# Performance work log

Hardware: AMD Instinct MI355X
Metric: run time of the kernel (lower is better)

## Reference

```python
import jax, jax.numpy as jnp
import numpy as np

N_NODES = 100000
N_EDGES = 1600000
IN_CH = 1024
FEAT_CH = 128
OUT_CH = 3


def setup_inputs() -> dict:
    key = jax.random.key(0)
    ks = jax.random.split(key, 9)
    features = jax.random.normal(ks[0], (N_NODES, IN_CH), dtype=jnp.float32)
    edges = jax.random.randint(ks[1], (2, N_EDGES), 0, N_NODES, dtype=jnp.int64)
    edges2 = jax.random.randint(ks[2], (2, N_EDGES), 0, N_NODES, dtype=jnp.int64)
    edge_features = jax.random.normal(ks[3], (N_EDGES, 1), dtype=jnp.float32)
    additional_feature = jax.random.normal(ks[4], (N_NODES, 20), dtype=jnp.float32)
    # GCNConv linear weights (glorot-ish scale) and biases
    W1 = jax.random.normal(ks[5], (IN_CH, FEAT_CH), dtype=jnp.float32) * (1.0 / np.sqrt(IN_CH))
    b1 = jnp.zeros((FEAT_CH,), dtype=jnp.float32)
    W2 = jax.random.normal(ks[6], (FEAT_CH, OUT_CH), dtype=jnp.float32) * (1.0 / np.sqrt(FEAT_CH))
    b2 = jnp.zeros((OUT_CH,), dtype=jnp.float32)
    return {"features": features, "edges": edges, "edges2": edges2,
            "edge_features": edge_features, "additional_feature": additional_feature,
            "W1": W1, "b1": b1, "W2": W2, "b2": b2}


def gcn_conv(x, edge_index, W, b, num_nodes):
    """PyG GCNConv: x' = D^{-1/2}(A+I)D^{-1/2} x W + b (self-loops added)."""
    x = x @ W  # project first (cheaper feature dim for aggregation)
    loop = jnp.arange(num_nodes, dtype=edge_index.dtype)
    src = jnp.concatenate([edge_index[0], loop])
    dst = jnp.concatenate([edge_index[1], loop])
    deg = jax.ops.segment_sum(jnp.ones_like(dst, dtype=x.dtype), dst,
                              num_segments=num_nodes)  # >=1 due to self-loops
    dinv = jax.lax.rsqrt(deg)
    norm = dinv[src] * dinv[dst]  # [E+N]
    out = jax.ops.segment_sum(x[src] * norm[:, None], dst, num_segments=num_nodes)
    return out + b


def reference(features, edges, edges2, edge_features, additional_feature, W1, b1, W2, b2):
    # use_additional_channels=False -> features unchanged; edge_features forced to None
    n = features.shape[0]
    x = gcn_conv(features, edges2, W1, b1, n)
    x = jax.nn.relu(x)
    # dropout inactive in eval mode
    return gcn_conv(x, edges2, W2, b2, n)
```

## Files before the change

kernel.cpp:

```cpp
#include <hip/hip_runtime.h>
#include <hip/hip_bf16.h>

typedef __attribute__((ext_vector_type(8))) _Float16 half8;
typedef __attribute__((ext_vector_type(4))) _Float16 half4;
typedef __attribute__((ext_vector_type(4))) float f32x4;

#define N_NODES 100000
#define N_EDGES 1600000
#define IN_CH 1024
#define FEAT 128
#define CAP 64
#define NDIG 196
#define CAPC 10240
#define MROWS 16
#define NGB (N_NODES / MROWS)

__device__ __forceinline__ int swzA(int row, int kbyte) {
    return row * 2048 + (kbyte ^ ((row & 7) << 4) ^ (((kbyte >> 8) & 7) << 4));
}

__global__ void k_prep(const float* __restrict__ W1, _Float16* __restrict__ Bf,
                       int* __restrict__ cursorC, int* __restrict__ done) {
    int idx = blockIdx.x * 256 + threadIdx.x;
    if (idx < IN_CH * FEAT) {
        int col = idx & (FEAT - 1), k = idx >> 7;
        int ct = col >> 4, ks = k >> 5;
        int lane = ((k >> 3) & 3) * 16 + (col & 15);
        int e = k & 7;
        Bf[(((ct * 32 + ks) * 64 + lane) << 3) + e] = (_Float16)W1[idx];
    }
    if (idx < NDIG) cursorC[idx] = idx * CAPC;
    if (idx == 0) *done = 0;
}

__global__ __launch_bounds__(256, 4) void k_build_gemm(
    const float* __restrict__ A, const _Float16* __restrict__ Bf,
    const int4* __restrict__ src4, const int4* __restrict__ dst4,
    int* __restrict__ cursorC, uint2* __restrict__ recs,
    int* __restrict__ csr, int* __restrict__ cnt, float* __restrict__ dinvarr,
    int* __restrict__ done, _Float16* __restrict__ H, int M, int e4)
{
    __shared__ union {
        _Float16 As[MROWS * IN_CH];
        struct { int hist[NDIG], segoff[NDIG], lcur[NDIG]; } bin;
        int cl[512];
    } sm;
    const int t = threadIdx.x;

    if (blockIdx.x < NDIG) {
        const int b = blockIdx.x;
        if (t < NDIG) sm.bin.hist[t] = 0;
        __syncthreads();
        const int base4 = b * 2048;
        int4 sv[8], dv[8];
#pragma unroll
        for (int j = 0; j < 8; ++j) {
            int idx = base4 + j * 256 + t;
            if (idx < e4) { sv[j] = src4[idx]; dv[j] = dst4[idx]; }
            else { sv[j] = (int4){-1,-1,-1,-1}; dv[j] = (int4){-1,-1,-1,-1}; }
        }
#pragma unroll
        for (int j = 0; j < 8; ++j) {
            int dd[4] = {dv[j].x, dv[j].y, dv[j].z, dv[j].w};
            int ss[4] = {sv[j].x, sv[j].y, sv[j].z, sv[j].w};
#pragma unroll
            for (int c = 0; c < 4; ++c)
                if ((unsigned)dd[c] < N_NODES && (unsigned)ss[c] < N_NODES)
                    atomicAdd(&sm.bin.hist[dd[c] >> 9], 1);
        }
        __syncthreads();
        if (t < NDIG) {
            sm.bin.segoff[t] = atomicAdd(&cursorC[t], sm.bin.hist[t]);
            sm.bin.lcur[t] = 0;
        }
        __syncthreads();
#pragma unroll
        for (int j = 0; j < 8; ++j) {
            int dd[4] = {dv[j].x, dv[j].y, dv[j].z, dv[j].w};
            int ss[4] = {sv[j].x, sv[j].y, sv[j].z, sv[j].w};
#pragma unroll
            for (int c = 0; c < 4; ++c) {
                if ((unsigned)dd[c] < N_NODES && (unsigned)ss[c] < N_NODES) {
                    int dg = dd[c] >> 9;
                    int r = atomicAdd(&sm.bin.lcur[dg], 1);
                    int pos = sm.bin.segoff[dg] + r;
                    if (pos < (dg + 1) * CAPC)
                        recs[pos] = (uint2){(unsigned)ss[c], (unsigned)dd[c]};
                }
            }
        }
        __syncthreads();
        if (t == 0) {
            __threadfence();
            __hip_atomic_fetch_add(done, 1, __ATOMIC_RELEASE, __HIP_MEMORY_SCOPE_AGENT);
            while (__hip_atomic_load(done, __ATOMIC_ACQUIRE, __HIP_MEMORY_SCOPE_AGENT) < NDIG)
                __builtin_amdgcn_s_sleep(8);
        }
        __syncthreads();
        const int d = blockIdx.x;
        for (int j = t; j < 512; j += 256) sm.cl[j] = 0;
        __syncthreads();
        const int base = d * CAPC;
        int n = cursorC[d] - base;
        if (n > CAPC) n = CAPC;
        for (int k = t; k < n; k += 256) {
            uint2 r = recs[base + k];
            int local = (int)r.y & 511;
            int slot = atomicAdd(&sm.cl[local], 1);
            if (slot < CAP) csr[((int)r.y << 6) + slot] = (int)r.x;
        }
        __syncthreads();
        const int node0 = d << 9;
        for (int j = t; j < 512; j += 256) {
            int node = node0 + j;
            if (node < N_NODES) {
                int c = sm.cl[j] < CAP ? sm.cl[j] : CAP;
                cnt[node] = c;
                dinvarr[node] = rsqrtf((float)(c + 1));
            }
        }
        return;
    }

    const int gb = blockIdx.x - NDIG;
    const int brow0 = gb * MROWS;
    const int wid = t >> 6, lane = t & 63;

    {
        const int row = t >> 4;
        const int c0 = (t & 15) * 64;
        const float* pa = A + (size_t)(brow0 + row) * IN_CH + c0;
        float4 v0[8], v1[8];
#pragma unroll
        for (int j = 0; j < 8; ++j) v0[j] = *(const float4*)(pa + j * 4);
#pragma unroll
        for (int j = 0; j < 8; ++j) v1[j] = *(const float4*)(pa + 32 + j * 4);
#pragma unroll
        for (int j = 0; j < 4; ++j) {
            half8 h;
            h[0] = (_Float16)v0[2 * j].x;     h[1] = (_Float16)v0[2 * j].y;
            h[2] = (_Float16)v0[2 * j].z;     h[3] = (_Float16)v0[2 * j].w;
            h[4] = (_Float16)v0[2 * j + 1].x; h[5] = (_Float16)v0[2 * j + 1].y;
            h[6] = (_Float16)v0[2 * j + 1].z; h[7] = (_Float16)v0[2 * j + 1].w;
            *(half8*)((char*)sm.As + swzA(row, c0 * 2 + j * 16)) = h;
        }
#pragma unroll
        for (int j = 0; j < 4; ++j) {
            half8 h;
            h[0] = (_Float16)v1[2 * j].x;     h[1] = (_Float16)v1[2 * j].y;
            h[2] = (_Float16)v1[2 * j].z;     h[3] = (_Float16)v1[2 * j].w;
            h[4] = (_Float16)v1[2 * j + 1].x; h[5] = (_Float16)v1[2 * j + 1].y;
            h[6] = (_Float16)v1[2 * j + 1].z; h[7] = (_Float16)v1[2 * j + 1].w;
            *(half8*)((char*)sm.As + swzA(row, (c0 + 32) * 2 + j * 16)) = h;
        }
    }
    __syncthreads();

    const int ct0 = wid * 2, ct1 = wid * 2 + 1;
    const _Float16* bfl = Bf + lane * 8;
    const _Float16* pb0 = bfl + ((size_t)(ct0 * 32) << 9);
    const _Float16* pb1 = bfl + ((size_t)(ct1 * 32) << 9);
    const int arow = lane & 15;
    const int asub = (lane >> 4) * 16;

    f32x4 acc0 = (f32x4){0.f, 0.f, 0.f, 0.f};
    f32x4 acc1 = (f32x4){0.f, 0.f, 0.f, 0.f};

    half8 bc0 = *(const half8*)(pb0);
    half8 bc1 = *(const half8*)(pb1);
#pragma unroll 4
    for (int ks = 0; ks < 32; ++ks) {
        half8 bn0 = bc0, bn1 = bc1;
        if (ks < 31) {
            bn0 = *(const half8*)(pb0 + ((size_t)(ks + 1) << 9));
            bn1 = *(const half8*)(pb1 + ((size_t)(ks + 1) << 9));
        }
        half8 a = *(const half8*)((char*)sm.As + swzA(arow, ks * 64 + asub));
        acc0 = __builtin_amdgcn_mfma_f32_16x16x32_f16(a, bc0, acc0, 0, 0, 0);
        acc1 = __builtin_amdgcn_mfma_f32_16x16x32_f16(a, bc1, acc1, 0, 0, 0);
        bc0 = bn0; bc1 = bn1;
    }

    {
        int colb = lane & 15, rgrp = (lane >> 4) * 4;
#pragma unroll
        for (int r = 0; r < 4; ++r) {
            int grow = brow0 + rgrp + r;
            _Float16* hp = H + (size_t)grow * FEAT;
            hp[ct0 * 16 + colb] = (_Float16)acc0[r];
            hp[ct1 * 16 + colb] = (_Float16)acc1[r];
        }
    }
}

__global__ __launch_bounds__(256) void k_agg1(const _Float16* __restrict__ H,
                                              const int* __restrict__ csr,
                                              const int* __restrict__ cnt,
                                              const float* __restrict__ dinvarr,
                                              const float* __restrict__ b1,
                                              const float* __restrict__ W2,
                                              float* __restrict__ Y, int n) {
    int wid = threadIdx.x >> 6, lane = threadIdx.x & 63;
    int i = blockIdx.x * 4 + wid;
    if (i >= n) return;
    const int g = lane >> 4, u = lane & 15;
    int m = cnt[i];
    float di = dinvarr[i];

    int sl; float dl;
    if (lane < m) { sl = csr[(i << 6) + lane]; dl = dinvarr[sl]; }
    else          { sl = i;                    dl = (lane == m) ? di : 0.f; }
    int mm = (m < 63 ? m : 63) + 1;

    float ax[8];
#pragma unroll
    for (int j = 0; j < 8; ++j) ax[j] = 0.f;

    for (int e = 0; e < mm; e += 16) {
        int idx0 = e + g, idx1 = e + 4 + g, idx2 = e + 8 + g, idx3 = e + 12 + g;
        bool v0 = idx0 < mm, v1 = idx1 < mm, v2 = idx2 < mm, v3 = idx3 < mm;
        int c0i = v0 ? idx0 : 0, c1i = v1 ? idx1 : 0;
        int c2i = v2 ? idx2 : 0, c3i = v3 ? idx3 : 0;
        int s0 = __shfl(sl, c0i); float w0 = __shfl(dl, c0i);
        int s1 = __shfl(sl, c1i); float w1 = __shfl(dl, c1i);
        int s2 = __shfl(sl, c2i); float w2 = __shfl(dl, c2i);
        int s3 = __shfl(sl, c3i); float w3 = __shfl(dl, c3i);
        if (!v0) { s0 = i; w0 = 0.f; }
        if (!v1) { s1 = i; w1 = 0.f; }
        if (!v2) { s2 = i; w2 = 0.f; }
        if (!v3) { s3 = i; w3 = 0.f; }
        half8 h0 = *(const half8*)(H + ((size_t)s0 << 7) + u * 8);
        half8 h1 = *(const half8*)(H + ((size_t)s1 << 7) + u * 8);
        half8 h2 = *(const half8*)(H + ((size_t)s2 << 7) + u * 8);
        half8 h3 = *(const half8*)(H + ((size_t)s3 << 7) + u * 8);
#pragma unroll
        for (int j = 0; j < 8; ++j)
            ax[j] += w0 * (float)h0[j] + w1 * (float)h1[j]
                   + w2 * (float)h2[j] + w3 * (float)h3[j];
    }

#pragma unroll
    for (int j = 0; j < 8; ++j) {
        ax[j] += __shfl_xor(ax[j], 16);
        ax[j] += __shfl_xor(ax[j], 32);
    }

    int c0 = u * 8;
    float y0 = 0.f, y1 = 0.f, y2 = 0.f;
#pragma unroll
    for (int j = 0; j < 8; ++j) {
        float x = di * ax[j] + b1[c0 + j];
        x = x > 0.f ? x : 0.f;
        y0 += x * W2[(c0 + j) * 3 + 0];
        y1 += x * W2[(c0 + j) * 3 + 1];
        y2 += x * W2[(c0 + j) * 3 + 2];
    }
#pragma unroll
    for (int d = 1; d < 16; d <<= 1) {
        y0 += __shfl_xor(y0, d);
        y1 += __shfl_xor(y1, d);
        y2 += __shfl_xor(y2, d);
    }
    if (lane == 0) {
        float* yp = Y + (size_t)i * 4;
        yp[0] = di * y0; yp[1] = di * y1; yp[2] = di * y2;
    }
}

__global__ void k_agg2(const float* __restrict__ Y, const int* __restrict__ csr,
                       const int* __restrict__ cnt, const float* __restrict__ dinvarr,
                       const float* __restrict__ b2, float* __restrict__ out, int n) {
    int i = blockIdx.x * 256 + threadIdx.x;
    if (i >= n) return;
    int m = cnt[i];
    float di = dinvarr[i];
    int base = i << 6;
    const float4* Y4 = (const float4*)Y;
    float4 self = Y4[i];
    float a0 = self.x, a1 = self.y, a2 = self.z;
    int e = 0;
    for (; e + 3 < m; e += 4) {
        int s0 = csr[base + e],     s1 = csr[base + e + 1];
        int s2 = csr[base + e + 2], s3 = csr[base + e + 3];
        float4 v0 = Y4[s0], v1 = Y4[s1], v2 = Y4[s2], v3 = Y4[s3];
        a0 += (v0.x + v1.x) + (v2.x + v3.x);
        a1 += (v0.y + v1.y) + (v2.y + v3.y);
        a2 += (v0.z + v1.z) + (v2.z + v3.z);
    }
    for (; e < m; ++e) {
        float4 v0 = Y4[csr[base + e]];
        a0 += v0.x; a1 += v0.y; a2 += v0.z;
    }
    out[(size_t)i * 3 + 0] = di * a0 + b2[0];
    out[(size_t)i * 3 + 1] = di * a1 + b2[1];
    out[(size_t)i * 3 + 2] = di * a2 + b2[2];
}

extern "C" void kernel_launch(void* const* d_in, const int* in_sizes, int n_in,
                              void* d_out, int out_size, void* d_ws, size_t ws_size,
                              hipStream_t stream) {
    const float* features = (const float*)d_in[0];
    const int* edges2 = (const int*)d_in[2];
    const float* W1 = (const float*)d_in[5];
    const float* b1 = (const float*)d_in[6];
    const float* W2 = (const float*)d_in[7];
    const float* b2 = (const float*)d_in[8];
    float* out = (float*)d_out;

    const int N = N_NODES, E = N_EDGES;
    const int4* src4 = (const int4*)edges2;
    const int4* dst4 = (const int4*)(edges2 + E);
    int e4 = E / 4;

    char* p = (char*)d_ws;
    auto carve = [&](size_t bytes) { char* q = p; p += (bytes + 255) & ~(size_t)255; return q; };
    int* cnt       = (int*)carve(4 * (size_t)N);
    float* dinvarr = (float*)carve(4 * (size_t)N);
    int* cursorC   = (int*)carve(4 * NDIG);
    int* done      = (int*)carve(4);
    uint2* recs    = (uint2*)carve(8 * (size_t)NDIG * CAPC);
    int* csr       = (int*)carve(4 * (size_t)N * CAP);
    _Float16* Bf   = (_Float16*)carve(2 * (size_t)IN_CH * FEAT);
    _Float16* H    = (_Float16*)carve(2 * (size_t)N * FEAT);
    float* Y       = (float*)carve(16 * (size_t)N);

    k_prep<<<dim3(512), dim3(256), 0, stream>>>(W1, Bf, cursorC, done);
    k_build_gemm<<<dim3(NDIG + NGB), dim3(256), 0, stream>>>(
        features, Bf, src4, dst4, cursorC, recs, csr, cnt, dinvarr, done, H, N, e4);
    k_agg1<<<dim3((N + 3) / 4), dim3(256), 0, stream>>>(H, csr, cnt, dinvarr, b1, W2, Y, N);
    k_agg2<<<dim3((N + 255) / 256), dim3(256), 0, stream>>>(Y, csr, cnt, dinvarr, b2, out, N);
}
```

Before: 297.2 us.

## Make GEMM blocks persistent with register-prefetched next panel and 32-row tiles

The fused build/GEMM kernel moves to 512-thread blocks. The GEMM part becomes a persistent grid of 512 blocks that loop over 32-row panels of the feature matrix, and the next panel's fp32 loads are issued into registers while MFMAs run on the current one. Each wave now computes one 16-column tile for two 16-row subtiles, so the B fragment is reused across rows rather than A across columns. The aim is to hide the latency of streaming the 400MB feature matrix and to cut per-block launch overhead. The cost is higher register pressure from 16 float4 prefetch registers and fewer blocks, which may reduce occupancy.

```diff
diff --git a/kernel.cpp b/kernel.cpp
--- a/kernel.cpp
+++ b/kernel.cpp
@@ -2,7 +2,6 @@
 #include <hip/hip_bf16.h>
 
 typedef __attribute__((ext_vector_type(8))) _Float16 half8;
-typedef __attribute__((ext_vector_type(4))) _Float16 half4;
 typedef __attribute__((ext_vector_type(4))) float f32x4;
 
 #define N_NODES 100000
@@ -12,8 +11,9 @@
 #define CAP 64
 #define NDIG 196
 #define CAPC 10240
-#define MROWS 16
-#define NGB (N_NODES / MROWS)
+#define MROWS 32
+#define NPAN (N_NODES / MROWS)
+#define NGBLK 512
 
 __device__ __forceinline__ int swzA(int row, int kbyte) {
     return row * 2048 + (kbyte ^ ((row & 7) << 4) ^ (((kbyte >> 8) & 7) << 4));
@@ -33,12 +33,12 @@
     if (idx == 0) *done = 0;
 }
 
-__global__ __launch_bounds__(256, 4) void k_build_gemm(
+__global__ __launch_bounds__(512, 4) void k_build_gemm(
     const float* __restrict__ A, const _Float16* __restrict__ Bf,
     const int4* __restrict__ src4, const int4* __restrict__ dst4,
     int* __restrict__ cursorC, uint2* __restrict__ recs,
     int* __restrict__ csr, int* __restrict__ cnt, float* __restrict__ dinvarr,
-    int* __restrict__ done, _Float16* __restrict__ H, int M, int e4)
+    int* __restrict__ done, _Float16* __restrict__ H, int e4)
 {
     __shared__ union {
         _Float16 As[MROWS * IN_CH];
@@ -52,15 +52,15 @@
         if (t < NDIG) sm.bin.hist[t] = 0;
         __syncthreads();
         const int base4 = b * 2048;
-        int4 sv[8], dv[8];
-#pragma unroll
-        for (int j = 0; j < 8; ++j) {
-            int idx = base4 + j * 256 + t;
+        int4 sv[4], dv[4];
+#pragma unroll
+        for (int j = 0; j < 4; ++j) {
+            int idx = base4 + j * 512 + t;
             if (idx < e4) { sv[j] = src4[idx]; dv[j] = dst4[idx]; }
             else { sv[j] = (int4){-1,-1,-1,-1}; dv[j] = (int4){-1,-1,-1,-1}; }
         }
 #pragma unroll
-        for (int j = 0; j < 8; ++j) {
+        for (int j = 0; j < 4; ++j) {
             int dd[4] = {dv[j].x, dv[j].y, dv[j].z, dv[j].w};
             int ss[4] = {sv[j].x, sv[j].y, sv[j].z, sv[j].w};
 #pragma unroll
@@ -75,7 +75,7 @@
         }
         __syncthreads();
 #pragma unroll
-        for (int j = 0; j < 8; ++j) {
+        for (int j = 0; j < 4; ++j) {
             int dd[4] = {dv[j].x, dv[j].y, dv[j].z, dv[j].w};
             int ss[4] = {sv[j].x, sv[j].y, sv[j].z, sv[j].w};
 #pragma unroll
@@ -98,12 +98,12 @@
         }
         __syncthreads();
         const int d = blockIdx.x;
-        for (int j = t; j < 512; j += 256) sm.cl[j] = 0;
+        if (t < 512) sm.cl[t] = 0;
         __syncthreads();
         const int base = d * CAPC;
         int n = cursorC[d] - base;
         if (n > CAPC) n = CAPC;
-        for (int k = t; k < n; k += 256) {
+        for (int k = t; k < n; k += 512) {
             uint2 r = recs[base + k];
             int local = (int)r.y & 511;
             int slot = atomicAdd(&sm.cl[local], 1);
@@ -111,10 +111,10 @@
         }
         __syncthreads();
         const int node0 = d << 9;
-        for (int j = t; j < 512; j += 256) {
-            int node = node0 + j;
-            if (node < N_NODES) {
-                int c = sm.cl[j] < CAP ? sm.cl[j] : CAP;
+        {
+            int node = node0 + t;
+            if (t < 512 && node < N_NODES) {
+                int c = sm.cl[t] < CAP ? sm.cl[t] : CAP;
                 cnt[node] = c;
                 dinvarr[node] = rsqrtf((float)(c + 1));
             }
@@ -122,75 +122,76 @@
         return;
     }
 
-    const int gb = blockIdx.x - NDIG;
-    const int brow0 = gb * MROWS;
+    const int gbase = blockIdx.x - NDIG;
     const int wid = t >> 6, lane = t & 63;
-
-    {
-        const int row = t >> 4;
-        const int c0 = (t & 15) * 64;
-        const float* pa = A + (size_t)(brow0 + row) * IN_CH + c0;
-        float4 v0[8], v1[8];
-#pragma unroll
-        for (int j = 0; j < 8; ++j) v0[j] = *(const float4*)(pa + j * 4);
-#pragma unroll
-        for (int j = 0; j < 8; ++j) v1[j] = *(const float4*)(pa + 32 + j * 4);
-#pragma unroll
-        for (int j = 0; j < 4; ++j) {
-            half8 h;
-            h[0] = (_Float16)v0[2 * j].x;     h[1] = (_Float16)v0[2 * j].y;
-            h[2] = (_Float16)v0[2 * j].z;     h[3] = (_Float16)v0[2 * j].w;
-            h[4] = (_Float16)v0[2 * j + 1].x; h[5] = (_Float16)v0[2 * j + 1].y;
-            h[6] = (_Float16)v0[2 * j + 1].z; h[7] = (_Float16)v0[2 * j + 1].w;
-            *(half8*)((char*)sm.As + swzA(row, c0 * 2 + j * 16)) = h;
-        }
-#pragma unroll
-        for (int j = 0; j < 4; ++j) {
-            half8 h;
-            h[0] = (_Float16)v1[2 * j].x;     h[1] = (_Float16)v1[2 * j].y;
-            h[2] = (_Float16)v1[2 * j].z;     h[3] = (_Float16)v1[2 * j].w;
-            h[4] = (_Float16)v1[2 * j + 1].x; h[5] = (_Float16)v1[2 * j + 1].y;
-            h[6] = (_Float16)v1[2 * j + 1].z; h[7] = (_Float16)v1[2 * j + 1].w;
-            *(half8*)((char*)sm.As + swzA(row, (c0 + 32) * 2 + j * 16)) = h;
-        }
-    }
-    __syncthreads();
-
-    const int ct0 = wid * 2, ct1 = wid * 2 + 1;
-    const _Float16* bfl = Bf + lane * 8;
-    const _Float16* pb0 = bfl + ((size_t)(ct0 * 32) << 9);
-    const _Float16* pb1 = bfl + ((size_t)(ct1 * 32) << 9);
+    const int ct = wid;
     const int arow = lane & 15;
     const int asub = (lane >> 4) * 16;
-
-    f32x4 acc0 = (f32x4){0.f, 0.f, 0.f, 0.f};
-    f32x4 acc1 = (f32x4){0.f, 0.f, 0.f, 0.f};
-
-    half8 bc0 = *(const half8*)(pb0);
-    half8 bc1 = *(const half8*)(pb1);
+    const _Float16* pbw = Bf + (((size_t)ct * 32) << 9) + lane * 8;
+
+    const int srow = t >> 4;
+    const int sc0 = (t & 15) * 64;
+
+    float4 sv[16];
+
+#define STAGE_LOAD(p)                                                           \
+    {                                                                           \
+        const float* pa_ = A + (size_t)((p) * MROWS + srow) * IN_CH + sc0;      \
+        _Pragma("unroll") for (int j = 0; j < 16; ++j)                          \
+            sv[j] = *(const float4*)(pa_ + j * 4);                              \
+    }
+#define CVT_WRITE()                                                             \
+    {                                                                           \
+        _Pragma("unroll") for (int j = 0; j < 8; ++j) {                         \
+            half8 h;                                                            \
+            h[0] = (_Float16)sv[2*j].x;   h[1] = (_Float16)sv[2*j].y;           \
+            h[2] = (_Float16)sv[2*j].z;   h[3] = (_Float16)sv[2*j].w;           \
+            h[4] = (_Float16)sv[2*j+1].x; h[5] = (_Float16)sv[2*j+1].y;         \
+            h[6] = (_Float16)sv[2*j+1].z; h[7] = (_Float16)sv[2*j+1].w;         \
+            *(half8*)((char*)sm.As + swzA(srow, sc0 * 2 + j * 16)) = h;         \
+        }                                                                       \
+    }
+
+    int p = gbase;
+    STAGE_LOAD(p);
+    CVT_WRITE();
+    __syncthreads();
+
+    for (;;) {
+        const int pn = p + NGBLK;
+        const bool more = (pn < NPAN);
+        if (more) STAGE_LOAD(pn);
+
+        f32x4 acc0 = (f32x4){0.f, 0.f, 0.f, 0.f};
+        f32x4 acc1 = (f32x4){0.f, 0.f, 0.f, 0.f};
+        half8 bc = *(const half8*)(pbw);
 #pragma unroll 4
-    for (int ks = 0; ks < 32; ++ks) {
-        half8 bn0 = bc0, bn1 = bc1;
-        if (ks < 31) {
-            bn0 = *(const half8*)(pb0 + ((size_t)(ks + 1) << 9));
-            bn1 = *(const half8*)(pb1 + ((size_t)(ks + 1) << 9));
-        }
-        half8 a = *(const half8*)((char*)sm.As + swzA(arow, ks * 64 + asub));
-        acc0 = __builtin_amdgcn_mfma_f32_16x16x32_f16(a, bc0, acc0, 0, 0, 0);
-        acc1 = __builtin_amdgcn_mfma_f32_16x16x32_f16(a, bc1, acc1, 0, 0, 0);
-        bc0 = bn0; bc1 = bn1;
-    }
-
-    {
-        int colb = lane & 15, rgrp = (lane >> 4) * 4;
-#pragma unroll
-        for (int r = 0; r < 4; ++r) {
-            int grow = brow0 + rgrp + r;
-            _Float16* hp = H + (size_t)grow * FEAT;
-            hp[ct0 * 16 + colb] = (_Float16)acc0[r];
-            hp[ct1 * 16 + colb] = (_Float16)acc1[r];
-        }
-    }
+        for (int ks = 0; ks < 32; ++ks) {
+            half8 bn = bc;
+            if (ks < 31) bn = *(const half8*)(pbw + ((size_t)(ks + 1) << 9));
+            half8 a0 = *(const half8*)((char*)sm.As + swzA(arow, ks * 64 + asub));
+            half8 a1 = *(const half8*)((char*)sm.As + swzA(16 + arow, ks * 64 + asub));
+            acc0 = __builtin_amdgcn_mfma_f32_16x16x32_f16(a0, bc, acc0, 0, 0, 0);
+            acc1 = __builtin_amdgcn_mfma_f32_16x16x32_f16(a1, bc, acc1, 0, 0, 0);
+            bc = bn;
+        }
+        {
+            const int brow0 = p * MROWS;
+            int colb = lane & 15, rgrp = (lane >> 4) * 4;
+#pragma unroll
+            for (int r = 0; r < 4; ++r) {
+                H[(size_t)(brow0 + rgrp + r) * FEAT + ct * 16 + colb] = (_Float16)acc0[r];
+                H[(size_t)(brow0 + 16 + rgrp + r) * FEAT + ct * 16 + colb] = (_Float16)acc1[r];
+            }
+        }
+        if (!more) break;
+        __syncthreads();
+        CVT_WRITE();
+        __syncthreads();
+        p = pn;
+    }
+#undef STAGE_LOAD
+#undef CVT_WRITE
 }
 
 __global__ __launch_bounds__(256) void k_agg1(const _Float16* __restrict__ H,
@@ -325,8 +326,8 @@
     float* Y       = (float*)carve(16 * (size_t)N);
 
     k_prep<<<dim3(512), dim3(256), 0, stream>>>(W1, Bf, cursorC, done);
-    k_build_gemm<<<dim3(NDIG + NGB), dim3(256), 0, stream>>>(
-        features, Bf, src4, dst4, cursorC, recs, csr, cnt, dinvarr, done, H, N, e4);
+    k_build_gemm<<<dim3(NDIG + NGBLK), dim3(512), 0, stream>>>(
+        features, Bf, src4, dst4, cursorC, recs, csr, cnt, dinvarr, done, H, e4);
     k_agg1<<<dim3((N + 3) / 4), dim3(256), 0, stream>>>(H, csr, cnt, dinvarr, b1, W2, Y, N);
     k_agg2<<<dim3((N + 255) / 256), dim3(256), 0, stream>>>(Y, csr, cnt, dinvarr, b2, out, N);
 }
```

Measured after the change: 310.3 us. 4.4% more time.
